# Kernel tuning notes

Hardware: AMD Instinct MI355X
Metric: run time of the kernel (lower is better)

The kernel has to match this reference:

```python
import jax, jax.numpy as jnp
import numpy as np

EMBED = 1024
HEADS = 16
HEAD_DIM = EMBED // HEADS


def setup_inputs() -> dict:
    key = jax.random.key(0)
    ks = jax.random.split(key, 8)
    N, L = 2, 2048
    values = jax.random.normal(ks[0], (N, L, EMBED), dtype=jnp.float32)
    keys_ = jax.random.normal(ks[1], (N, L, EMBED), dtype=jnp.float32)
    query = jax.random.normal(ks[2], (N, L, EMBED), dtype=jnp.float32)
    mask = jnp.ones((N, 1, 1, L), dtype=jnp.int32)
    s = 1.0 / np.sqrt(EMBED)
    W_q = jax.random.normal(ks[3], (EMBED, EMBED), dtype=jnp.float32) * s
    W_k = jax.random.normal(ks[4], (EMBED, EMBED), dtype=jnp.float32) * s
    W_v = jax.random.normal(ks[5], (EMBED, EMBED), dtype=jnp.float32) * s
    W_o = jax.random.normal(ks[6], (EMBED, EMBED), dtype=jnp.float32) * s
    b_o = jax.random.normal(ks[7], (EMBED,), dtype=jnp.float32) * 0.01
    return {"values": values, "keys": keys_, "query": query, "mask": mask,
            "W_q": W_q, "W_k": W_k, "W_v": W_v, "W_o": W_o, "b_o": b_o}


def reference(values, keys, query, mask, W_q, W_k, W_v, W_o, b_o):
    N, Lq, _ = query.shape
    Lk = keys.shape[1]
    # projections (torch Linear: x @ W.T); reshape to (N, H, L, Dh)
    q = (query @ W_q.T).reshape(N, Lq, HEADS, HEAD_DIM).transpose(0, 2, 1, 3)
    k = (keys @ W_k.T).reshape(N, Lk, HEADS, HEAD_DIM).transpose(0, 2, 1, 3)
    v = (values @ W_v.T).reshape(N, Lk, HEADS, HEAD_DIM).transpose(0, 2, 1, 3)
    energy = jnp.einsum('bhqd,bhkd->bhqk', q, k) / jnp.sqrt(jnp.float32(HEAD_DIM))
    energy = jnp.where(mask == 0, jnp.float32(-1e20), energy)
    attn = jax.nn.softmax(energy, axis=-1)
    out = jnp.einsum('bhqk,bhkd->bhqd', attn, v)
    out = out.transpose(0, 2, 1, 3).reshape(N, Lq, EMBED)
    return out @ W_o.T + b_o
```

## Files before the change

### kernel.cpp

```cpp
#include <hip/hip_runtime.h>
#include <cstddef>
#include <cstdint>

#define SEQ    2048
#define NBATCH 2

typedef unsigned short u16;
typedef unsigned int   u32;
typedef __attribute__((ext_vector_type(8))) short bf16x8;
typedef __attribute__((ext_vector_type(4))) short bf16x4;
typedef __attribute__((ext_vector_type(4))) float f32x4;

#if __has_builtin(__builtin_amdgcn_exp2f)
#define EXP2F(x) __builtin_amdgcn_exp2f(x)
#else
#define EXP2F(x) exp2f(x)
#endif

#define MFMA_K16(a, b, c) __builtin_amdgcn_mfma_f32_16x16x16bf16_1k(a, b, c, 0, 0, 0)

__device__ __forceinline__ u32 fbits(float x) { union { float f; u32 u; } c; c.f = x; return c.u; }
__device__ __forceinline__ u16 f2bf(float x) { return (u16)((fbits(x) + 0x8000u) >> 16); }
__device__ __forceinline__ u32 pack2bf(float lo, float hi) {
    return __builtin_amdgcn_perm(fbits(hi) + 0x8000u, fbits(lo) + 0x8000u, 0x07060302u);
}
__device__ __forceinline__ bf16x4 mk_bf16x4(u32 lo, u32 hi) {
    union { u32 w[2]; bf16x4 v; } u; u.w[0] = lo; u.w[1] = hi; return u.v;
}

__global__ __launch_bounds__(256)
void cast3(const float* __restrict__ a, const float* __restrict__ b, const float* __restrict__ c,
           u16* __restrict__ oa, u16* __restrict__ ob, u16* __restrict__ oc, int n4)
{
    const float* s; u16* d;
    if (blockIdx.y == 0)      { s = a; d = oa; }
    else if (blockIdx.y == 1) { s = b; d = ob; }
    else                      { s = c; d = oc; }
    int i = blockIdx.x * 256 + threadIdx.x;
    if (i >= n4) return;
    float4 v = ((const float4*)s)[i];
    uint2 r; r.x = pack2bf(v.x, v.y); r.y = pack2bf(v.z, v.w);
    ((uint2*)d)[i] = r;
}

__global__ __launch_bounds__(256)
void cast4(const float* __restrict__ a, const float* __restrict__ b,
           const float* __restrict__ c, const float* __restrict__ e,
           u16* __restrict__ oa, u16* __restrict__ ob, u16* __restrict__ oc, u16* __restrict__ oe,
           int n4)
{
    const float* s; u16* d;
    if (blockIdx.y == 0)      { s = a; d = oa; }
    else if (blockIdx.y == 1) { s = b; d = ob; }
    else if (blockIdx.y == 2) { s = c; d = oc; }
    else                      { s = e; d = oe; }
    int i = blockIdx.x * 256 + threadIdx.x;
    if (i >= n4) return;
    float4 v = ((const float4*)s)[i];
    uint2 r; r.x = pack2bf(v.x, v.y); r.y = pack2bf(v.z, v.w);
    ((uint2*)d)[i] = r;
}

__device__ __forceinline__
void gemm_body(const u16* __restrict__ X, const u16* __restrict__ W,
               void* __restrict__ Yv, const int layout)
{
    __shared__ u16 smem[2 * 128 * 72];
    u16* As = smem;
    u16* Bs = smem + 128 * 72;

    const int tid  = threadIdx.x;
    const int wave = tid >> 6;
    const int lane = tid & 63;
    const int lm   = lane & 15;
    const int quad = lane >> 4;
    const int m0 = blockIdx.x * 128;
    const int n0 = blockIdx.y * 128;
    const int wr = (wave & 1) * 64;
    const int wc = (wave >> 1) * 64;

    const int srow = tid >> 1;
    const int scol = (tid & 1) * 32;
    const u16* xg = X + (size_t)(m0 + srow) * 1024 + scol;
    const u16* wg = W + (size_t)(n0 + srow) * 1024 + scol;

    bf16x8 pa[4], pb[4];
    #pragma unroll
    for (int p = 0; p < 4; ++p) {
        pa[p] = *(const bf16x8*)(xg + p * 8);
        pb[p] = *(const bf16x8*)(wg + p * 8);
    }

    f32x4 acc[4][4] = {};

    for (int k0 = 0; k0 < 1024; k0 += 64) {
        __syncthreads();
        #pragma unroll
        for (int p = 0; p < 4; ++p) {
            *(bf16x8*)&As[srow * 72 + scol + p * 8] = pa[p];
            *(bf16x8*)&Bs[srow * 72 + scol + p * 8] = pb[p];
        }
        __syncthreads();
        if (k0 + 64 < 1024) {
            #pragma unroll
            for (int p = 0; p < 4; ++p) {
                pa[p] = *(const bf16x8*)(xg + k0 + 64 + p * 8);
                pb[p] = *(const bf16x8*)(wg + k0 + 64 + p * 8);
            }
        }
        #pragma unroll
        for (int kk = 0; kk < 64; kk += 32) {
            bf16x8 af[4], bf[4];
            #pragma unroll
            for (int t = 0; t < 4; ++t) {
                af[t] = *(const bf16x8*)&As[(wr + t * 16 + lm) * 72 + kk + quad * 8];
                bf[t] = *(const bf16x8*)&Bs[(wc + t * 16 + lm) * 72 + kk + quad * 8];
            }
            #pragma unroll
            for (int i = 0; i < 4; ++i)
                #pragma unroll
                for (int j = 0; j < 4; ++j)
                    acc[i][j] = __builtin_amdgcn_mfma_f32_16x16x32_bf16(af[i], bf[j], acc[i][j], 0, 0, 0);
        }
    }

    if (layout == 0) {
        u16* Y = (u16*)Yv;
        #pragma unroll
        for (int i = 0; i < 4; ++i)
            #pragma unroll
            for (int j = 0; j < 4; ++j) {
                const int C = n0 + wc + j * 16 + lm;
                #pragma unroll
                for (int r = 0; r < 4; ++r) {
                    const int R = m0 + wr + i * 16 + quad * 4 + r;
                    Y[(size_t)R * 1024 + C] = f2bf(acc[i][j][r]);
                }
            }
    } else {
        __syncthreads();
        u16* T = smem;
        #pragma unroll
        for (int i = 0; i < 4; ++i)
            #pragma unroll
            for (int j = 0; j < 4; ++j) {
                const int col = wc + j * 16 + lm;
                const int row = wr + i * 16 + quad * 4;
                uint2 v;
                v.x = pack2bf(acc[i][j][0], acc[i][j][1]);
                v.y = pack2bf(acc[i][j][2], acc[i][j][3]);
                *(uint2*)&T[col * 132 + row] = v;
            }
        __syncthreads();
        const int dp = tid >> 1, half = (tid & 1) * 64;
        const int nn = m0 >> 11, l0 = m0 & 2047;
        const int C = n0 + dp, h = C >> 6, d = C & 63;
        u16* Y = (u16*)Yv;
        const size_t base = (((size_t)nn * 16 + h) * 64 + d) * SEQ + l0 + half;
        #pragma unroll
        for (int p = 0; p < 8; ++p) {
            bf16x8 v = *(const bf16x8*)&T[dp * 132 + half + p * 8];
            *(bf16x8*)(Y + base + p * 8) = v;
        }
    }
}

__global__ __launch_bounds__(256, 2)
void gemm_qkv(const u16* __restrict__ xq, const u16* __restrict__ xk, const u16* __restrict__ xv,
              const u16* __restrict__ wq, const u16* __restrict__ wk, const u16* __restrict__ wv,
              u16* __restrict__ qb, u16* __restrict__ kb, u16* __restrict__ vt)
{
    if (blockIdx.z == 0)      gemm_body(xq, wq, qb, 0);
    else if (blockIdx.z == 1) gemm_body(xk, wk, kb, 0);
    else                      gemm_body(xv, wv, vt, 2);
}

__global__ __launch_bounds__(256, 2)
void gemm_out64(const u16* __restrict__ X, const u16* __restrict__ W,
                float* __restrict__ Y, const float* __restrict__ bias)
{
    __shared__ u16 As[128 * 72];
    __shared__ u16 Bs[64 * 72];

    const int tid  = threadIdx.x;
    const int wave = tid >> 6;
    const int lane = tid & 63;
    const int lm   = lane & 15;
    const int quad = lane >> 4;
    const int m0 = blockIdx.x * 128;
    const int n0 = blockIdx.y * 64;
    const int wr = (wave & 1) * 64;
    const int wc = (wave >> 1) * 32;

    const int arow = tid >> 1, acol = (tid & 1) * 32;
    const int brow = tid >> 2, bcol = (tid & 3) * 16;
    const u16* xg = X + (size_t)(m0 + arow) * 1024 + acol;
    const u16* wg = W + (size_t)(n0 + brow) * 1024 + bcol;

    bf16x8 pa[4], pb[2];
    #pragma unroll
    for (int p = 0; p < 4; ++p) pa[p] = *(const bf16x8*)(xg + p * 8);
    #pragma unroll
    for (int p = 0; p < 2; ++p) pb[p] = *(const bf16x8*)(wg + p * 8);

    f32x4 acc[4][2] = {};

    for (int k0 = 0; k0 < 1024; k0 += 64) {
        __syncthreads();
        #pragma unroll
        for (int p = 0; p < 4; ++p) *(bf16x8*)&As[arow * 72 + acol + p * 8] = pa[p];
        #pragma unroll
        for (int p = 0; p < 2; ++p) *(bf16x8*)&Bs[brow * 72 + bcol + p * 8] = pb[p];
        __syncthreads();
        if (k0 + 64 < 1024) {
            #pragma unroll
            for (int p = 0; p < 4; ++p) pa[p] = *(const bf16x8*)(xg + k0 + 64 + p * 8);
            #pragma unroll
            for (int p = 0; p < 2; ++p) pb[p] = *(const bf16x8*)(wg + k0 + 64 + p * 8);
        }
        #pragma unroll
        for (int kk = 0; kk < 64; kk += 32) {
            bf16x8 af[4], bf[2];
            #pragma unroll
            for (int t = 0; t < 4; ++t)
                af[t] = *(const bf16x8*)&As[(wr + t * 16 + lm) * 72 + kk + quad * 8];
            #pragma unroll
            for (int j = 0; j < 2; ++j)
                bf[j] = *(const bf16x8*)&Bs[(wc + j * 16 + lm) * 72 + kk + quad * 8];
            #pragma unroll
            for (int i = 0; i < 4; ++i)
                #pragma unroll
                for (int j = 0; j < 2; ++j)
                    acc[i][j] = __builtin_amdgcn_mfma_f32_16x16x32_bf16(af[i], bf[j], acc[i][j], 0, 0, 0);
        }
    }

    #pragma unroll
    for (int i = 0; i < 4; ++i)
        #pragma unroll
        for (int j = 0; j < 2; ++j) {
            const int C = n0 + wc + j * 16 + lm;
            const float bv = bias[C];
            #pragma unroll
            for (int r = 0; r < 4; ++r) {
                const int R = m0 + wr + i * 16 + quad * 4 + r;
                Y[(size_t)R * 1024 + C] = acc[i][j][r] + bv;
            }
        }
}

__global__ __launch_bounds__(256, 2)
void flash_attn_bf16(const u16* __restrict__ Qb, const u16* __restrict__ Kb,
                     const u16* __restrict__ VT, const int* __restrict__ mask,
                     u16* __restrict__ O)
{
    __shared__ u16 Ks[128 * 72];
    __shared__ u16 Vts[64 * 136];

    const int tid  = threadIdx.x;
    const int wave = tid >> 6;
    const int lane = tid & 63;
    const int lm   = lane & 15;
    const int quad = lane >> 4;
    const int h = blockIdx.y, n = blockIdx.z;
    const int wq = blockIdx.x * 128 + wave * 32;

    const u16* Qh = Qb + ((size_t)n * SEQ) * 1024 + h * 64;
    const u16* Kh = Kb + ((size_t)n * SEQ) * 1024 + h * 64;
    const u16* Vh = VT + (((size_t)n * 16 + h) * 64) * SEQ;
    const int* mk = mask + (size_t)n * SEQ;

    bf16x8 qf[2][2];
    #pragma unroll
    for (int qt = 0; qt < 2; ++qt)
        #pragma unroll
        for (int ks = 0; ks < 2; ++ks)
            qf[qt][ks] = *(const bf16x8*)(Qh + (size_t)(wq + qt * 16 + lm) * 1024 + ks * 32 + quad * 8);

    f32x4 o_acc[2][4] = {};
    float l_i[2] = {};

    const int kr = tid >> 1, kc = (tid & 1) * 32;
    const int vr = tid >> 2, vc = (tid & 3) * 32;

    bf16x8 ka[4], va[4];
    #pragma unroll
    for (int p = 0; p < 4; ++p) {
        ka[p] = *(const bf16x8*)(Kh + (size_t)kr * 1024 + kc + p * 8);
        va[p] = *(const bf16x8*)(Vh + (size_t)vr * SEQ + vc + p * 8);
    }

    const float cs = 0.125f * 1.44269504f;

    for (int c0 = 0; c0 < SEQ; c0 += 128) {
        __syncthreads();
        #pragma unroll
        for (int p = 0; p < 4; ++p) {
            *(bf16x8*)&Ks[kr * 72 + kc + p * 8]   = ka[p];
            *(bf16x8*)&Vts[vr * 136 + vc + p * 8] = va[p];
        }
        __syncthreads();

        if (c0 + 128 < SEQ) {
            #pragma unroll
            for (int p = 0; p < 4; ++p) {
                ka[p] = *(const bf16x8*)(Kh + (size_t)(c0 + 128 + kr) * 1024 + kc + p * 8);
                va[p] = *(const bf16x8*)(Vh + (size_t)vr * SEQ + c0 + 128 + vc + p * 8);
            }
        }

        int4 mkv[8];
        #pragma unroll
        for (int kt = 0; kt < 8; ++kt)
            mkv[kt] = *(const int4*)(mk + c0 + kt * 16 + quad * 4);

        f32x4 st[8][2] = {};
        #pragma unroll
        for (int kt = 0; kt < 8; ++kt) {
            bf16x8 kf0 = *(const bf16x8*)&Ks[(kt * 16 + lm) * 72 + quad * 8];
            bf16x8 kf1 = *(const bf16x8*)&Ks[(kt * 16 + lm) * 72 + 32 + quad * 8];
            #pragma unroll
            for (int qt = 0; qt < 2; ++qt) {
                st[kt][qt] = __builtin_amdgcn_mfma_f32_16x16x32_bf16(kf0, qf[qt][0], st[kt][qt], 0, 0, 0);
                st[kt][qt] = __builtin_amdgcn_mfma_f32_16x16x32_bf16(kf1, qf[qt][1], st[kt][qt], 0, 0, 0);
            }
        }

        bf16x4 pf[8][2];
        #pragma unroll
        for (int kt = 0; kt < 8; ++kt) {
            const int4 mv = mkv[kt];
            const int mm[4] = {mv.x, mv.y, mv.z, mv.w};
            #pragma unroll
            for (int qt = 0; qt < 2; ++qt) {
                float e[4];
                #pragma unroll
                for (int r = 0; r < 4; ++r) {
                    float v = EXP2F(st[kt][qt][r] * cs);
                    v = mm[r] ? v : 0.0f;
                    e[r] = v;
                    l_i[qt] += v;
                }
                pf[kt][qt] = mk_bf16x4(pack2bf(e[0], e[1]), pack2bf(e[2], e[3]));
            }
        }

        #pragma unroll
        for (int kt = 0; kt < 8; ++kt)
            #pragma unroll
            for (int dt = 0; dt < 4; ++dt) {
                bf16x4 vf = *(const bf16x4*)&Vts[(dt * 16 + lm) * 136 + kt * 16 + quad * 4];
                #pragma unroll
                for (int qt = 0; qt < 2; ++qt)
                    o_acc[qt][dt] = MFMA_K16(pf[kt][qt], vf, o_acc[qt][dt]);
            }
    }

    float linv[2][4];
    #pragma unroll
    for (int qt = 0; qt < 2; ++qt) {
        float v = l_i[qt];
        v += __shfl_xor(v, 16);
        v += __shfl_xor(v, 32);
        #pragma unroll
        for (int r = 0; r < 4; ++r)
            linv[qt][r] = 1.0f / __shfl(v, quad * 4 + r);
    }
    #pragma unroll
    for (int qt = 0; qt < 2; ++qt)
        #pragma unroll
        for (int dt = 0; dt < 4; ++dt)
            #pragma unroll
            for (int r = 0; r < 4; ++r) {
                const int ql = wq + qt * 16 + quad * 4 + r;
                const int col = h * 64 + dt * 16 + lm;
                O[((size_t)n * SEQ + ql) * 1024 + col] = f2bf(o_acc[qt][dt][r] * linv[qt][r]);
            }
}

extern "C" void kernel_launch(void* const* d_in, const int* in_sizes, int n_in,
                              void* d_out, int out_size, void* d_ws, size_t ws_size,
                              hipStream_t stream)
{
    const float* values = (const float*)d_in[0];
    const float* keys   = (const float*)d_in[1];
    const float* query  = (const float*)d_in[2];
    const int*   mask   = (const int*)d_in[3];
    const float* W_q    = (const float*)d_in[4];
    const float* W_k    = (const float*)d_in[5];
    const float* W_v    = (const float*)d_in[6];
    const float* W_o    = (const float*)d_in[7];
    const float* b_o    = (const float*)d_in[8];

    const size_t NTOK = (size_t)NBATCH * SEQ * 1024;
    const size_t WSZ  = 1024 * 1024;
    u16* p = (u16*)d_ws;
    u16* qb    = p; p += NTOK;
    u16* kb    = p; p += NTOK;
    u16* vt    = p; p += NTOK;
    u16* xq    = p; p += NTOK;
    u16* xk    = p; p += NTOK;
    u16* xv    = p; p += NTOK;
    u16* attnb = p; p += NTOK;
    u16* wqb   = p; p += WSZ;
    u16* wkb   = p; p += WSZ;
    u16* wvb   = p; p += WSZ;
    u16* wob   = p; p += WSZ;

    cast3<<<dim3(4096, 3), 256, 0, stream>>>(query, keys, values, xq, xk, xv, (int)(NTOK / 4));
    cast4<<<dim3(1024, 4), 256, 0, stream>>>(W_q, W_k, W_v, W_o, wqb, wkb, wvb, wob, (int)(WSZ / 4));

    gemm_qkv<<<dim3(32, 8, 3), 256, 0, stream>>>(xq, xk, xv, wqb, wkb, wvb, qb, kb, vt);

    flash_attn_bf16<<<dim3(16, 16, 2), 256, 0, stream>>>(qb, kb, vt, mask, attnb);

    gemm_out64<<<dim3(32, 16), 256, 0, stream>>>(attnb, wob, (float*)d_out, b_o);
}
```

Baseline: 237.1 us.

## Merge cast kernels, remap attention blocks, and route P through LDS for K32 MFMA

Merges the activation and weight bf16 cast kernels into one launch, which saves a kernel launch. Raises the occupancy hint on the QKV GEMM. In attention, it remaps block indices so that blocks sharing a head and batch are grouped, and swaps the QK^T operand order so each lane owns per-row sums. It also writes the probabilities P to a per-wave LDS buffer so the PV product can use 16x16x32 MFMAs in place of 16x16x16, at the cost of extra LDS traffic and shared memory.

```diff
diff --git a/kernel.cpp b/kernel.cpp
--- a/kernel.cpp
+++ b/kernel.cpp
@@ -8,7 +8,6 @@
 typedef unsigned short u16;
 typedef unsigned int   u32;
 typedef __attribute__((ext_vector_type(8))) short bf16x8;
-typedef __attribute__((ext_vector_type(4))) short bf16x4;
 typedef __attribute__((ext_vector_type(4))) float f32x4;
 
 #if __has_builtin(__builtin_amdgcn_exp2f)
@@ -17,47 +16,34 @@
 #define EXP2F(x) exp2f(x)
 #endif
 
-#define MFMA_K16(a, b, c) __builtin_amdgcn_mfma_f32_16x16x16bf16_1k(a, b, c, 0, 0, 0)
-
 __device__ __forceinline__ u32 fbits(float x) { union { float f; u32 u; } c; c.f = x; return c.u; }
 __device__ __forceinline__ u16 f2bf(float x) { return (u16)((fbits(x) + 0x8000u) >> 16); }
 __device__ __forceinline__ u32 pack2bf(float lo, float hi) {
     return __builtin_amdgcn_perm(fbits(hi) + 0x8000u, fbits(lo) + 0x8000u, 0x07060302u);
 }
-__device__ __forceinline__ bf16x4 mk_bf16x4(u32 lo, u32 hi) {
-    union { u32 w[2]; bf16x4 v; } u; u.w[0] = lo; u.w[1] = hi; return u.v;
-}
 
 __global__ __launch_bounds__(256)
-void cast3(const float* __restrict__ a, const float* __restrict__ b, const float* __restrict__ c,
-           u16* __restrict__ oa, u16* __restrict__ ob, u16* __restrict__ oc, int n4)
-{
-    const float* s; u16* d;
-    if (blockIdx.y == 0)      { s = a; d = oa; }
-    else if (blockIdx.y == 1) { s = b; d = ob; }
-    else                      { s = c; d = oc; }
-    int i = blockIdx.x * 256 + threadIdx.x;
-    if (i >= n4) return;
-    float4 v = ((const float4*)s)[i];
-    uint2 r; r.x = pack2bf(v.x, v.y); r.y = pack2bf(v.z, v.w);
-    ((uint2*)d)[i] = r;
-}
-
-__global__ __launch_bounds__(256)
-void cast4(const float* __restrict__ a, const float* __restrict__ b,
-           const float* __restrict__ c, const float* __restrict__ e,
-           u16* __restrict__ oa, u16* __restrict__ ob, u16* __restrict__ oc, u16* __restrict__ oe,
-           int n4)
-{
-    const float* s; u16* d;
-    if (blockIdx.y == 0)      { s = a; d = oa; }
-    else if (blockIdx.y == 1) { s = b; d = ob; }
-    else if (blockIdx.y == 2) { s = c; d = oc; }
-    else                      { s = e; d = oe; }
-    int i = blockIdx.x * 256 + threadIdx.x;
-    if (i >= n4) return;
-    float4 v = ((const float4*)s)[i];
-    uint2 r; r.x = pack2bf(v.x, v.y); r.y = pack2bf(v.z, v.w);
+void cast_all(const float* __restrict__ q, const float* __restrict__ k, const float* __restrict__ v,
+              const float* __restrict__ wq, const float* __restrict__ wk,
+              const float* __restrict__ wv, const float* __restrict__ wo,
+              u16* __restrict__ oq, u16* __restrict__ ok, u16* __restrict__ ov,
+              u16* __restrict__ owq, u16* __restrict__ owk, u16* __restrict__ owv,
+              u16* __restrict__ owo)
+{
+    const float* s; u16* d; int i;
+    if (blockIdx.y == 0)      { s = q; d = oq; i = blockIdx.x * 256 + threadIdx.x; }
+    else if (blockIdx.y == 1) { s = k; d = ok; i = blockIdx.x * 256 + threadIdx.x; }
+    else if (blockIdx.y == 2) { s = v; d = ov; i = blockIdx.x * 256 + threadIdx.x; }
+    else {
+        const int w = blockIdx.x >> 10, xi = blockIdx.x & 1023;
+        if (w == 0)      { s = wq; d = owq; }
+        else if (w == 1) { s = wk; d = owk; }
+        else if (w == 2) { s = wv; d = owv; }
+        else             { s = wo; d = owo; }
+        i = xi * 256 + threadIdx.x;
+    }
+    float4 vv = ((const float4*)s)[i];
+    uint2 r; r.x = pack2bf(vv.x, vv.y); r.y = pack2bf(vv.z, vv.w);
     ((uint2*)d)[i] = r;
 }
 
@@ -165,7 +151,7 @@
     }
 }
 
-__global__ __launch_bounds__(256, 2)
+__global__ __launch_bounds__(256, 3)
 void gemm_qkv(const u16* __restrict__ xq, const u16* __restrict__ xk, const u16* __restrict__ xv,
               const u16* __restrict__ wq, const u16* __restrict__ wk, const u16* __restrict__ wv,
               u16* __restrict__ qb, u16* __restrict__ kb, u16* __restrict__ vt)
@@ -256,29 +242,35 @@
 {
     __shared__ u16 Ks[128 * 72];
     __shared__ u16 Vts[64 * 136];
+    __shared__ u16 Ps[4][32 * 72];
 
     const int tid  = threadIdx.x;
     const int wave = tid >> 6;
     const int lane = tid & 63;
     const int lm   = lane & 15;
     const int quad = lane >> 4;
-    const int h = blockIdx.y, n = blockIdx.z;
-    const int wq = blockIdx.x * 128 + wave * 32;
+
+    const int wid = blockIdx.x + 16 * blockIdx.y + 256 * blockIdx.z;
+    const int idx = wid >> 3;
+    const int hn  = (wid & 7) + 8 * (idx & 3);
+    const int h   = hn & 15, n = hn >> 4;
+    const int wq  = (idx >> 2) * 128 + wave * 32;
 
     const u16* Qh = Qb + ((size_t)n * SEQ) * 1024 + h * 64;
     const u16* Kh = Kb + ((size_t)n * SEQ) * 1024 + h * 64;
     const u16* Vh = VT + (((size_t)n * 16 + h) * 64) * SEQ;
     const int* mk = mask + (size_t)n * SEQ;
+    u16* Pw = &Ps[wave][0];
 
     bf16x8 qf[2][2];
     #pragma unroll
-    for (int qt = 0; qt < 2; ++qt)
-        #pragma unroll
-        for (int ks = 0; ks < 2; ++ks)
-            qf[qt][ks] = *(const bf16x8*)(Qh + (size_t)(wq + qt * 16 + lm) * 1024 + ks * 32 + quad * 8);
+    for (int t = 0; t < 2; ++t)
+        #pragma unroll
+        for (int s = 0; s < 2; ++s)
+            qf[t][s] = *(const bf16x8*)(Qh + (size_t)(wq + t * 16 + lm) * 1024 + s * 32 + quad * 8);
 
     f32x4 o_acc[2][4] = {};
-    float l_i[2] = {};
+    float l_i[2][4] = {};
 
     const int kr = tid >> 1, kc = (tid & 1) * 32;
     const int vr = tid >> 2, vc = (tid & 3) * 32;
@@ -309,72 +301,79 @@
             }
         }
 
-        int4 mkv[8];
-        #pragma unroll
-        for (int kt = 0; kt < 8; ++kt)
-            mkv[kt] = *(const int4*)(mk + c0 + kt * 16 + quad * 4);
-
-        f32x4 st[8][2] = {};
-        #pragma unroll
-        for (int kt = 0; kt < 8; ++kt) {
-            bf16x8 kf0 = *(const bf16x8*)&Ks[(kt * 16 + lm) * 72 + quad * 8];
-            bf16x8 kf1 = *(const bf16x8*)&Ks[(kt * 16 + lm) * 72 + 32 + quad * 8];
-            #pragma unroll
-            for (int qt = 0; qt < 2; ++qt) {
-                st[kt][qt] = __builtin_amdgcn_mfma_f32_16x16x32_bf16(kf0, qf[qt][0], st[kt][qt], 0, 0, 0);
-                st[kt][qt] = __builtin_amdgcn_mfma_f32_16x16x32_bf16(kf1, qf[qt][1], st[kt][qt], 0, 0, 0);
-            }
-        }
-
-        bf16x4 pf[8][2];
-        #pragma unroll
-        for (int kt = 0; kt < 8; ++kt) {
-            const int4 mv = mkv[kt];
-            const int mm[4] = {mv.x, mv.y, mv.z, mv.w};
-            #pragma unroll
-            for (int qt = 0; qt < 2; ++qt) {
-                float e[4];
+        f32x4 s[2][8] = {};
+        #pragma unroll
+        for (int nt = 0; nt < 8; ++nt) {
+            bf16x8 kf0 = *(const bf16x8*)&Ks[(nt * 16 + lm) * 72 + quad * 8];
+            bf16x8 kf1 = *(const bf16x8*)&Ks[(nt * 16 + lm) * 72 + 32 + quad * 8];
+            #pragma unroll
+            for (int t = 0; t < 2; ++t) {
+                s[t][nt] = __builtin_amdgcn_mfma_f32_16x16x32_bf16(qf[t][0], kf0, s[t][nt], 0, 0, 0);
+                s[t][nt] = __builtin_amdgcn_mfma_f32_16x16x32_bf16(qf[t][1], kf1, s[t][nt], 0, 0, 0);
+            }
+        }
+
+        int msk[8];
+        #pragma unroll
+        for (int nt = 0; nt < 8; ++nt) msk[nt] = mk[c0 + nt * 16 + lm];
+        #pragma unroll
+        for (int t = 0; t < 2; ++t)
+            #pragma unroll
+            for (int nt = 0; nt < 8; ++nt)
                 #pragma unroll
                 for (int r = 0; r < 4; ++r) {
-                    float v = EXP2F(st[kt][qt][r] * cs);
-                    v = mm[r] ? v : 0.0f;
-                    e[r] = v;
-                    l_i[qt] += v;
+                    float e = EXP2F(s[t][nt][r] * cs);
+                    e = msk[nt] ? e : 0.0f;
+                    s[t][nt][r] = e;
+                    l_i[t][r] += e;
                 }
-                pf[kt][qt] = mk_bf16x4(pack2bf(e[0], e[1]), pack2bf(e[2], e[3]));
-            }
-        }
-
-        #pragma unroll
-        for (int kt = 0; kt < 8; ++kt)
-            #pragma unroll
-            for (int dt = 0; dt < 4; ++dt) {
-                bf16x4 vf = *(const bf16x4*)&Vts[(dt * 16 + lm) * 136 + kt * 16 + quad * 4];
-                #pragma unroll
-                for (int qt = 0; qt < 2; ++qt)
-                    o_acc[qt][dt] = MFMA_K16(pf[kt][qt], vf, o_acc[qt][dt]);
-            }
-    }
-
-    float linv[2][4];
-    #pragma unroll
-    for (int qt = 0; qt < 2; ++qt) {
-        float v = l_i[qt];
-        v += __shfl_xor(v, 16);
-        v += __shfl_xor(v, 32);
-        #pragma unroll
-        for (int r = 0; r < 4; ++r)
-            linv[qt][r] = 1.0f / __shfl(v, quad * 4 + r);
-    }
-    #pragma unroll
-    for (int qt = 0; qt < 2; ++qt)
+
+        #pragma unroll
+        for (int half = 0; half < 2; ++half) {
+            #pragma unroll
+            for (int t = 0; t < 2; ++t)
+                #pragma unroll
+                for (int ntl = 0; ntl < 4; ++ntl)
+                    #pragma unroll
+                    for (int r = 0; r < 4; ++r)
+                        Pw[(t * 16 + quad * 4 + r) * 72 + ntl * 16 + lm] =
+                            f2bf(s[t][half * 4 + ntl][r]);
+
+            #pragma unroll
+            for (int ksl = 0; ksl < 2; ++ksl) {
+                bf16x8 pf[2];
+                #pragma unroll
+                for (int t = 0; t < 2; ++t)
+                    pf[t] = *(const bf16x8*)&Pw[(t * 16 + lm) * 72 + ksl * 32 + quad * 8];
+                #pragma unroll
+                for (int dt = 0; dt < 4; ++dt) {
+                    bf16x8 vf = *(const bf16x8*)&Vts[(dt * 16 + lm) * 136 + half * 64 + ksl * 32 + quad * 8];
+                    #pragma unroll
+                    for (int t = 0; t < 2; ++t)
+                        o_acc[t][dt] = __builtin_amdgcn_mfma_f32_16x16x32_bf16(pf[t], vf, o_acc[t][dt], 0, 0, 0);
+                }
+            }
+        }
+    }
+
+    #pragma unroll
+    for (int t = 0; t < 2; ++t)
+        #pragma unroll
+        for (int r = 0; r < 4; ++r) {
+            float v = l_i[t][r];
+            #pragma unroll
+            for (int off = 1; off < 16; off <<= 1) v += __shfl_xor(v, off);
+            l_i[t][r] = 1.0f / v;
+        }
+    #pragma unroll
+    for (int t = 0; t < 2; ++t)
         #pragma unroll
         for (int dt = 0; dt < 4; ++dt)
             #pragma unroll
             for (int r = 0; r < 4; ++r) {
-                const int ql = wq + qt * 16 + quad * 4 + r;
+                const int ql = wq + t * 16 + quad * 4 + r;
                 const int col = h * 64 + dt * 16 + lm;
-                O[((size_t)n * SEQ + ql) * 1024 + col] = f2bf(o_acc[qt][dt][r] * linv[qt][r]);
+                O[((size_t)n * SEQ + ql) * 1024 + col] = f2bf(o_acc[t][dt][r] * l_i[t][r]);
             }
 }
 
@@ -407,8 +406,9 @@
     u16* wvb   = p; p += WSZ;
     u16* wob   = p; p += WSZ;
 
-    cast3<<<dim3(4096, 3), 256, 0, stream>>>(query, keys, values, xq, xk, xv, (int)(NTOK / 4));
-    cast4<<<dim3(1024, 4), 256, 0, stream>>>(W_q, W_k, W_v, W_o, wqb, wkb, wvb, wob, (int)(WSZ / 4));
+    cast_all<<<dim3(4096, 4), 256, 0, stream>>>(query, keys, values,
+                                                W_q, W_k, W_v, W_o,
+                                                xq, xk, xv, wqb, wkb, wvb, wob);
 
     gemm_qkv<<<dim3(32, 8, 3), 256, 0, stream>>>(xq, xk, xv, wqb, wkb, wvb, qb, kb, vt);
 
```

Result: faster. 228.9 us (-3.5%).
